# Kernel tuning notes

Measured on AMD Instinct MI355X. Metric: run time of the kernel, lower is better.

The kernel has to match this reference:

```python
import jax, jax.numpy as jnp
import numpy as np

N_NODES = 50000
N_EDGES = 10000
NNZ = 1600000
IN_DIM = 256
OUT_DIM = 128


def setup_inputs() -> dict:
    key = jax.random.key(0)
    k1, k2, k3, k4, k5 = jax.random.split(key, 5)
    X = jax.random.normal(k1, (N_NODES, IN_DIM), dtype=jnp.float32)
    theta = jax.random.normal(k2, (IN_DIM, OUT_DIM), dtype=jnp.float32) * (1.0 / np.sqrt(IN_DIM))
    bias = jax.random.normal(k3, (OUT_DIM,), dtype=jnp.float32) * 0.01
    node_idx = jax.random.randint(k4, (NNZ,), 0, N_NODES, dtype=jnp.int32)
    hyedge_idx = jax.random.randint(k5, (NNZ,), 0, N_EDGES, dtype=jnp.int32)
    return {
        "X": X,
        "theta": theta,
        "bias": bias,
        "node_idx": node_idx,
        "hyedge_idx": hyedge_idx,
        "num_nodes": N_NODES,
        "num_edges": N_EDGES,
    }


def reference(X, theta, bias, node_idx, hyedge_idx, num_nodes, num_edges):
    # Dense transform: [N, in] @ [in, out] -> [N, out]
    Xt = X @ theta
    # MA_v: vertex -> hyperedge aggregation (gather by node_idx, scatter_add by hyedge_idx)
    Y = jax.ops.segment_sum(Xt[node_idx], hyedge_idx, num_segments=num_edges)  # [M, out]
    # MA_e: hyperedge -> vertex aggregation (gather by hyedge_idx, scatter_add by node_idx)
    X_new = jax.ops.segment_sum(Y[hyedge_idx], node_idx, num_segments=num_nodes)  # [N, out]
    # U_v: bias add
    return X_new + bias
```

## Files before the change

### kernel.cpp

```cpp
#include <hip/hip_runtime.h>
#include <hip/hip_bf16.h>

#define NN 50000
#define NE 10000
#define KD 256
#define MD 128

#define NCAP 76

#define RNG 4
#define RDIV 12500
#define ERCAP 96

#define NB_E 313
#define NB_N 196
#define NBT  (NB_E + NB_N)
#define CCAP_E 5760
#define CCAP_N 8960

#define GEMM_BLKS ((NN + 255) / 256)
#define NCB 256
#define CSPAN 6252
#define CPB 6272
#define VIT 4

typedef __attribute__((ext_vector_type(8))) short short8;
typedef __attribute__((ext_vector_type(4))) float f32x4;

union ABfrag { short8 s; unsigned u[4]; };

__device__ inline unsigned pack_bf2(float a, float b) {
    __hip_bfloat162 h = __float22bfloat162_rn(make_float2(a, b));
    return *reinterpret_cast<unsigned*>(&h);
}

__device__ inline unsigned short bf16_1(float a) {
    __hip_bfloat16 h = __float2bfloat16(a);
    return *reinterpret_cast<unsigned short*>(&h);
}

__device__ inline float bf_lo(unsigned v) { return __uint_as_float(v << 16); }
__device__ inline float bf_hi(unsigned v) { return __uint_as_float(v & 0xffff0000u); }

__device__ inline void exscan_block(const int* __restrict__ cnt, int* __restrict__ lst,
                                    int n, int* buf, int tid) {
    int v = (tid < n) ? cnt[tid] : 0;
    buf[tid] = v;
    __syncthreads();
    #pragma unroll
    for (int s = 1; s < 512; s <<= 1) {
        int t = (tid >= s) ? buf[tid - s] : 0;
        __syncthreads();
        buf[tid] += t;
        __syncthreads();
    }
    if (tid < n) lst[tid] = buf[tid] - v;
    __syncthreads();
}

__global__ __launch_bounds__(256) void prep_theta(const float* __restrict__ Th,
                                                  unsigned short* __restrict__ tT,
                                                  int* __restrict__ ccur) {
    int tid = threadIdx.x;
    if (blockIdx.x == 0) { ccur[tid] = 0; ccur[tid + 256] = 0; }
    int gid = blockIdx.x * 256 + tid;
    int k = gid >> 7, c = gid & 127;
    tT[(size_t)c * KD + k] = bf16_1(Th[(size_t)k * MD + c]);
}

__global__ __launch_bounds__(512) void gemm_coarse(const float* __restrict__ X,
                                                   const unsigned short* __restrict__ tT,
                                                   unsigned short* __restrict__ XtU, int N,
                                                   const int* __restrict__ nidx,
                                                   const int* __restrict__ eidx,
                                                   int* __restrict__ ccur,
                                                   unsigned* __restrict__ coarse_e,
                                                   unsigned* __restrict__ coarse_n, int nnz) {
    __shared__ unsigned srt[CPB];
    __shared__ int cnt[NBT], lst[NBT], gb[NBT];
    __shared__ int wsum[8], wpre[8];
    const int tid = threadIdx.x;
    const int wv = tid >> 6, lane = tid & 63;

    if (blockIdx.x >= NCB) {
        const int lr = lane & 15;
        const int lk = lane >> 4;
        const int row0 = (blockIdx.x - NCB) * 256 + wv * 32;
        const int rowA = row0 + lr;
        const int rowB = row0 + 16 + lr;

        f32x4 acc0[8], acc1[8];
        #pragma unroll
        for (int ct = 0; ct < 8; ++ct) {
            acc0[ct] = (f32x4){0.f, 0.f, 0.f, 0.f};
            acc1[ct] = (f32x4){0.f, 0.f, 0.f, 0.f};
        }

        const short8* tTv = (const short8*)tT;
        #pragma unroll
        for (int ks = 0; ks < 8; ++ks) {
            ABfrag a0, a1;
            if (rowA < N) {
                const float* xp = X + (size_t)rowA * KD + ks * 32 + lk * 8;
                float4 v0 = *(const float4*)(xp);
                float4 v1 = *(const float4*)(xp + 4);
                a0.u[0] = pack_bf2(v0.x, v0.y);
                a0.u[1] = pack_bf2(v0.z, v0.w);
                a0.u[2] = pack_bf2(v1.x, v1.y);
                a0.u[3] = pack_bf2(v1.z, v1.w);
            } else a0.u[0] = a0.u[1] = a0.u[2] = a0.u[3] = 0u;
            if (rowB < N) {
                const float* xp = X + (size_t)rowB * KD + ks * 32 + lk * 8;
                float4 v0 = *(const float4*)(xp);
                float4 v1 = *(const float4*)(xp + 4);
                a1.u[0] = pack_bf2(v0.x, v0.y);
                a1.u[1] = pack_bf2(v0.z, v0.w);
                a1.u[2] = pack_bf2(v1.x, v1.y);
                a1.u[3] = pack_bf2(v1.z, v1.w);
            } else a1.u[0] = a1.u[1] = a1.u[2] = a1.u[3] = 0u;

            #pragma unroll
            for (int ct = 0; ct < 8; ++ct) {
                ABfrag b;
                b.s = tTv[(size_t)(ct * 16 + lr) * 32 + ks * 4 + lk];
                acc0[ct] = __builtin_amdgcn_mfma_f32_16x16x32_bf16(a0.s, b.s, acc0[ct], 0, 0, 0);
                acc1[ct] = __builtin_amdgcn_mfma_f32_16x16x32_bf16(a1.s, b.s, acc1[ct], 0, 0, 0);
            }
        }

        #pragma unroll
        for (int ct = 0; ct < 8; ++ct) {
            #pragma unroll
            for (int i = 0; i < 4; ++i) {
                int rA = row0 + lk * 4 + i;
                int rB = row0 + 16 + lk * 4 + i;
                if (rA < N) XtU[(size_t)rA * MD + ct * 16 + lr] = bf16_1(acc0[ct][i]);
                if (rB < N) XtU[(size_t)rB * MD + ct * 16 + lr] = bf16_1(acc1[ct][i]);
            }
        }
        return;
    }

    const int k0 = blockIdx.x * CSPAN;
    int k1 = k0 + CSPAN; if (k1 > nnz) k1 = nnz;
    const int nk = (k1 > k0) ? (k1 - k0) : 0;

    for (int j = tid; j < NBT; j += 512) cnt[j] = 0;
    __syncthreads();

    const int4* e4 = (const int4*)(eidx + k0);
    const int4* n4 = (const int4*)(nidx + k0);
    unsigned rr[VIT * 4];
    #pragma unroll
    for (int it = 0; it < VIT; ++it) {
        int vi = tid + it * 512;
        int base = vi * 4;
        int4 ev = make_int4(0, 0, 0, 0), nv = make_int4(0, 0, 0, 0);
        if (base < nk) { ev = e4[vi]; nv = n4[vi]; }
        #pragma unroll
        for (int j = 0; j < 4; ++j) {
            int e = (j == 0) ? ev.x : (j == 1) ? ev.y : (j == 2) ? ev.z : ev.w;
            int n = (j == 0) ? nv.x : (j == 1) ? nv.y : (j == 2) ? nv.z : nv.w;
            unsigned r = 0u;
            if (base + j < nk) {
                r = ((unsigned)n << 14) | (unsigned)e;
                atomicAdd(&cnt[e >> 5], 1);
                atomicAdd(&cnt[NB_E + (n >> 8)], 1);
            }
            rr[it * 4 + j] = r;
        }
    }
    __syncthreads();

    {
        int myv = (tid < NBT) ? cnt[tid] : 0;
        int v = myv;
        #pragma unroll
        for (int s = 1; s < 64; s <<= 1) {
            int t = __shfl_up(v, s);
            if (lane >= s) v += t;
        }
        if (lane == 63) wsum[wv] = v;
        __syncthreads();
        if (wv == 0) {
            int u = (lane < 8) ? wsum[lane] : 0;
            #pragma unroll
            for (int s = 1; s < 8; s <<= 1) {
                int t = __shfl_up(u, s);
                if (lane >= s) u += t;
            }
            if (lane < 8) wpre[lane] = u - wsum[lane];
        }
        __syncthreads();
        if (tid < NBT) lst[tid] = v - myv + wpre[wv];
        __syncthreads();
    }

    for (int j = tid; j < NBT; j += 512) {
        int c = cnt[j];
        gb[j] = c ? atomicAdd(&ccur[j], c) : 0;
        cnt[j] = 0;
    }
    __syncthreads();

    #pragma unroll
    for (int it = 0; it < VIT; ++it) {
        #pragma unroll
        for (int j = 0; j < 4; ++j) {
            int i = (tid + it * 512) * 4 + j;
            if (i < nk) {
                unsigned r = rr[it * 4 + j];
                int b = (r & 0x3FFF) >> 5;
                int rk = atomicAdd(&cnt[b], 1);
                srt[lst[b] + rk] = r;
            }
        }
    }
    __syncthreads();
    for (int p = tid; p < nk; p += 512) {
        unsigned r = srt[p];
        int b = (r & 0x3FFF) >> 5;
        int g = gb[b] + (p - lst[b]);
        if (g < CCAP_E) coarse_e[(size_t)b * CCAP_E + g] = r;
    }
    __syncthreads();

    #pragma unroll
    for (int it = 0; it < VIT; ++it) {
        #pragma unroll
        for (int j = 0; j < 4; ++j) {
            int i = (tid + it * 512) * 4 + j;
            if (i < nk) {
                unsigned r = rr[it * 4 + j];
                int b = NB_E + ((int)(r >> 14) >> 8);
                int rk = atomicAdd(&cnt[b], 1);
                srt[(lst[b] - nk) + rk] = r;
            }
        }
    }
    __syncthreads();
    for (int p = tid; p < nk; p += 512) {
        unsigned r = srt[p];
        int b = NB_E + ((int)(r >> 14) >> 8);
        int g = gb[b] + (p - (lst[b] - nk));
        if (g < CCAP_N) coarse_n[(size_t)(b - NB_E) * CCAP_N + g] = r;
    }
}

__global__ __launch_bounds__(512) void fine_e(const unsigned* __restrict__ coarse_e,
                                              const int* __restrict__ ccur,
                                              unsigned short* __restrict__ e_slots,
                                              int* __restrict__ e_cnt) {
    __shared__ unsigned srt[CCAP_E];
    __shared__ int cnt[128], lst[128];
    const int tid = threadIdx.x;
    const int b = blockIdx.x;

    const unsigned* buf = coarse_e + (size_t)b * CCAP_E;
    int m = ccur[b]; if (m > CCAP_E) m = CCAP_E;

    for (int j = tid; j < 128; j += 512) cnt[j] = 0;
    __syncthreads();
    for (int i = tid; i < m; i += 512) {
        unsigned r = buf[i];
        int e = r & 0x3FFF;
        int n = (int)(r >> 14);
        atomicAdd(&cnt[((e & 31) << 2) | (n / RDIV)], 1);
    }
    __syncthreads();
    exscan_block(cnt, lst, 128, (int*)srt, tid);
    if (tid < 128) {
        int e = b * 32 + (tid >> 2);
        if (e < NE) {
            int c = cnt[tid]; if (c > ERCAP) c = ERCAP;
            e_cnt[e * RNG + (tid & 3)] = c;
        }
    }
    __syncthreads();
    for (int j = tid; j < 128; j += 512) cnt[j] = 0;
    __syncthreads();
    for (int i = tid; i < m; i += 512) {
        unsigned r = buf[i];
        int e = r & 0x3FFF;
        unsigned n = r >> 14;
        int li = ((e & 31) << 2) | ((int)n / RDIV);
        int rk = atomicAdd(&cnt[li], 1);
        srt[lst[li] + rk] = ((unsigned)li << 16) | n;
    }
    __syncthreads();
    for (int p = tid; p < m; p += 512) {
        unsigned v = srt[p];
        int li = (int)(v >> 16);
        int lr = p - lst[li];
        if (lr < ERCAP) {
            int e = b * 32 + (li >> 2);
            e_slots[((size_t)e * RNG + (li & 3)) * ERCAP + lr] = (unsigned short)(v & 0xFFFF);
        }
    }
}

#define AGG_BLKS ((NE + 7) / 8 * RNG)

__global__ __launch_bounds__(512) void fine_n_agg_ve(const unsigned* __restrict__ coarse_n,
                                                     const int* __restrict__ ccur,
                                                     unsigned short* __restrict__ n_slots,
                                                     int* __restrict__ n_cnt,
                                                     const unsigned* __restrict__ XtB,
                                                     const int* __restrict__ e_cnt,
                                                     const unsigned short* __restrict__ e_slots,
                                                     unsigned* __restrict__ P) {
    __shared__ unsigned srt[CCAP_N];
    __shared__ int cnt[256], lst[256];
    const int tid = threadIdx.x;

    if (blockIdx.x < NB_N) {
        const int bb = blockIdx.x;
        const unsigned* buf = coarse_n + (size_t)bb * CCAP_N;
        int m = ccur[NB_E + bb]; if (m > CCAP_N) m = CCAP_N;

        for (int j = tid; j < 256; j += 512) cnt[j] = 0;
        __syncthreads();
        for (int i = tid; i < m; i += 512) {
            unsigned r = buf[i];
            atomicAdd(&cnt[(r >> 14) & 255], 1);
        }
        __syncthreads();
        exscan_block(cnt, lst, 256, (int*)srt, tid);
        if (tid < 256) {
            int g = bb * 256 + tid;
            if (g < NN) {
                int c = cnt[tid]; if (c > NCAP) c = NCAP;
                n_cnt[g] = c;
            }
        }
        __syncthreads();
        for (int j = tid; j < 256; j += 512) cnt[j] = 0;
        __syncthreads();
        for (int i = tid; i < m; i += 512) {
            unsigned r = buf[i];
            int k = (r >> 14) & 255;
            int rk = atomicAdd(&cnt[k], 1);
            srt[lst[k] + rk] = ((unsigned)k << 16) | (r & 0x3FFF);
        }
        __syncthreads();
        for (int p = tid; p < m; p += 512) {
            unsigned v = srt[p];
            int k = (int)(v >> 16);
            int lr = p - lst[k];
            if (lr < NCAP) {
                int g = bb * 256 + k;
                n_slots[(size_t)g * NCAP + lr] = (unsigned short)(v & 0x3FFF);
            }
        }
        return;
    }

    const int wid = blockIdx.x - NB_N;
    const int r = wid & 3;
    const int g = wid >> 2;
    int wave = g * 8 + (tid >> 6);
    int l    = tid & 63;
    const int grp = l >> 3, sub = l & 7;
    int ec = e_cnt[wave * RNG + r]; if (ec > ERCAP) ec = ERCAP;
    const unsigned short* slots = e_slots + ((size_t)wave * RNG + r) * ERCAP;
    const uint4* Xv = (const uint4*)XtB;

    float a[16];
    #pragma unroll
    for (int i = 0; i < 16; ++i) a[i] = 0.f;

    for (int c = 0; c < ec; c += 64) {
        int m = ec - c; if (m > 64) m = 64;
        int idx = (c + l < ec) ? (int)slots[c + l] : 0;
        for (int j = 0; j < m; j += 8) {
            int mem = j + grp;
            bool valid = mem < m;
            int n = __shfl(idx, valid ? mem : 0);
            const uint4* row = Xv + (size_t)n * 16 + sub * 2;
            uint4 v0 = row[0];
            uint4 v1 = row[1];
            if (valid) {
                a[0]  += bf_lo(v0.x); a[1]  += bf_hi(v0.x);
                a[2]  += bf_lo(v0.y); a[3]  += bf_hi(v0.y);
                a[4]  += bf_lo(v0.z); a[5]  += bf_hi(v0.z);
                a[6]  += bf_lo(v0.w); a[7]  += bf_hi(v0.w);
                a[8]  += bf_lo(v1.x); a[9]  += bf_hi(v1.x);
                a[10] += bf_lo(v1.y); a[11] += bf_hi(v1.y);
                a[12] += bf_lo(v1.z); a[13] += bf_hi(v1.z);
                a[14] += bf_lo(v1.w); a[15] += bf_hi(v1.w);
            }
        }
    }
    #pragma unroll
    for (int i = 0; i < 16; ++i) {
        a[i] += __shfl_xor(a[i], 8);
        a[i] += __shfl_xor(a[i], 16);
        a[i] += __shfl_xor(a[i], 32);
    }
    if (l < 8) {
        uint4 o0 = make_uint4(pack_bf2(a[0],  a[1]),  pack_bf2(a[2],  a[3]),
                              pack_bf2(a[4],  a[5]),  pack_bf2(a[6],  a[7]));
        uint4 o1 = make_uint4(pack_bf2(a[8],  a[9]),  pack_bf2(a[10], a[11]),
                              pack_bf2(a[12], a[13]), pack_bf2(a[14], a[15]));
        uint4* prow = (uint4*)P + ((size_t)r * NE + wave) * 16 + sub * 2;
        prow[0] = o0;
        prow[1] = o1;
    }
}

__global__ __launch_bounds__(256) void reduce_y(const unsigned* __restrict__ P,
                                                unsigned* __restrict__ YB) {
    int gid = blockIdx.x * 256 + threadIdx.x;
    if (gid >= NE * 64) return;
    float a = 0.f, b = 0.f;
    #pragma unroll
    for (int r = 0; r < RNG; ++r) {
        unsigned v = P[(size_t)r * NE * 64 + gid];
        a += bf_lo(v);
        b += bf_hi(v);
    }
    YB[gid] = pack_bf2(a, b);
}

__global__ __launch_bounds__(256) void agg_ev(const unsigned* __restrict__ YB,
                                              const int* __restrict__ n_cnt,
                                              const unsigned short* __restrict__ n_slots,
                                              const float* __restrict__ bias,
                                              float* __restrict__ out) {
    int wave = blockIdx.x * 4 + (threadIdx.x >> 6);
    int l    = threadIdx.x & 63;
    if (wave >= NN) return;
    const int grp = l >> 3, sub = l & 7;
    int cnt = n_cnt[wave]; if (cnt > NCAP) cnt = NCAP;
    const unsigned short* slots = n_slots + (size_t)wave * NCAP;
    const uint4* Yv = (const uint4*)YB;

    float a[16];
    #pragma unroll
    for (int i = 0; i < 16; ++i) a[i] = 0.f;

    for (int c = 0; c < cnt; c += 64) {
        int m = cnt - c; if (m > 64) m = 64;
        int idx = (c + l < cnt) ? (int)slots[c + l] : 0;
        for (int j = 0; j < m; j += 8) {
            int mem = j + grp;
            bool valid = mem < m;
            int e = __shfl(idx, valid ? mem : 0);
            const uint4* row = Yv + (size_t)e * 16 + sub * 2;
            uint4 v0 = row[0];
            uint4 v1 = row[1];
            if (valid) {
                a[0]  += bf_lo(v0.x); a[1]  += bf_hi(v0.x);
                a[2]  += bf_lo(v0.y); a[3]  += bf_hi(v0.y);
                a[4]  += bf_lo(v0.z); a[5]  += bf_hi(v0.z);
                a[6]  += bf_lo(v0.w); a[7]  += bf_hi(v0.w);
                a[8]  += bf_lo(v1.x); a[9]  += bf_hi(v1.x);
                a[10] += bf_lo(v1.y); a[11] += bf_hi(v1.y);
                a[12] += bf_lo(v1.z); a[13] += bf_hi(v1.z);
                a[14] += bf_lo(v1.w); a[15] += bf_hi(v1.w);
            }
        }
    }
    #pragma unroll
    for (int i = 0; i < 16; ++i) {
        a[i] += __shfl_xor(a[i], 8);
        a[i] += __shfl_xor(a[i], 16);
        a[i] += __shfl_xor(a[i], 32);
    }
    if (l < 8) {
        float4* orow = (float4*)(out + (size_t)wave * MD);
        #pragma unroll
        for (int q = 0; q < 4; ++q) {
            float4 bq = ((const float4*)bias)[sub * 4 + q];
            float4 o = make_float4(a[q * 4 + 0] + bq.x, a[q * 4 + 1] + bq.y,
                                   a[q * 4 + 2] + bq.z, a[q * 4 + 3] + bq.w);
            orow[sub * 4 + q] = o;
        }
    }
}

extern "C" void kernel_launch(void* const* d_in, const int* in_sizes, int n_in,
                              void* d_out, int out_size, void* d_ws, size_t ws_size,
                              hipStream_t stream) {
    const float* X     = (const float*)d_in[0];
    const float* theta = (const float*)d_in[1];
    const float* bias  = (const float*)d_in[2];
    const int*   nidx  = (const int*)d_in[3];
    const int*   eidx  = (const int*)d_in[4];
    float*       out   = (float*)d_out;

    const int N   = in_sizes[0] / KD;
    const int nnz = in_sizes[3];

    char* w = (char*)d_ws;
    unsigned*       XtB      = (unsigned*)w;       w += (size_t)NN * MD * 2;
    unsigned*       YB       = (unsigned*)w;       w += (size_t)NE * MD * 2;
    int*            e_cnt    = (int*)w;            w += (size_t)NE * RNG * 4;
    int*            n_cnt    = (int*)w;            w += (size_t)NN * 4;
    int*            ccur     = (int*)w;            w += (size_t)512 * 4;
    unsigned short* thetaT   = (unsigned short*)w; w += (size_t)MD * KD * 2;
    unsigned*       P        = (unsigned*)w;       w += (size_t)RNG * NE * 64 * 4;
    unsigned*       coarse_e = (unsigned*)w;       w += (size_t)NB_E * CCAP_E * 4;
    unsigned*       coarse_n = (unsigned*)w;       w += (size_t)NB_N * CCAP_N * 4;
    unsigned short* e_slots  = (unsigned short*)w; w += (size_t)NE * RNG * ERCAP * 2;
    unsigned short* n_slots  = (unsigned short*)w;

    prep_theta<<<(MD * KD) / 256, 256, 0, stream>>>(theta, thetaT, ccur);

    gemm_coarse<<<NCB + GEMM_BLKS, 512, 0, stream>>>(X, thetaT, (unsigned short*)XtB, N,
                                                     nidx, eidx, ccur,
                                                     coarse_e, coarse_n, nnz);

    fine_e<<<NB_E, 512, 0, stream>>>(coarse_e, ccur, e_slots, e_cnt);

    fine_n_agg_ve<<<NB_N + AGG_BLKS, 512, 0, stream>>>(coarse_n, ccur, n_slots, n_cnt,
                                                       XtB, e_cnt, e_slots, P);

    reduce_y<<<(NE * 64 + 255) / 256, 256, 0, stream>>>(P, YB);

    agg_ev<<<(NN + 3) / 4, 256, 0, stream>>>(YB, n_cnt, n_slots, bias, out);
}
```

Measured before the change: 125.2 us.

## Move node-side coarse binning into the fine_e kernel to rebalance stages

```diff
diff --git a/kernel.cpp b/kernel.cpp
--- a/kernel.cpp
+++ b/kernel.cpp
@@ -24,6 +24,8 @@
 #define CPB 6272
 #define VIT 4
 
+#define AGG_BLKS ((NE + 7) / 8 * RNG)
+
 typedef __attribute__((ext_vector_type(8))) short short8;
 typedef __attribute__((ext_vector_type(4))) float f32x4;
 
@@ -55,6 +57,31 @@
         __syncthreads();
     }
     if (tid < n) lst[tid] = buf[tid] - v;
+    __syncthreads();
+}
+
+__device__ inline void wave_exscan(const int* __restrict__ cnt, int* __restrict__ lst,
+                                   int n, int* wsum, int* wpre, int tid, int wv, int lane) {
+    int myv = (tid < n) ? cnt[tid] : 0;
+    int v = myv;
+    #pragma unroll
+    for (int s = 1; s < 64; s <<= 1) {
+        int t = __shfl_up(v, s);
+        if (lane >= s) v += t;
+    }
+    if (lane == 63) wsum[wv] = v;
+    __syncthreads();
+    if (wv == 0) {
+        int u = (lane < 8) ? wsum[lane] : 0;
+        #pragma unroll
+        for (int s = 1; s < 8; s <<= 1) {
+            int t = __shfl_up(u, s);
+            if (lane >= s) u += t;
+        }
+        if (lane < 8) wpre[lane] = u - wsum[lane];
+    }
+    __syncthreads();
+    if (tid < n) lst[tid] = v - myv + wpre[wv];
     __syncthreads();
 }
 
@@ -68,16 +95,15 @@
     tT[(size_t)c * KD + k] = bf16_1(Th[(size_t)k * MD + c]);
 }
 
-__global__ __launch_bounds__(512) void gemm_coarse(const float* __restrict__ X,
-                                                   const unsigned short* __restrict__ tT,
-                                                   unsigned short* __restrict__ XtU, int N,
-                                                   const int* __restrict__ nidx,
-                                                   const int* __restrict__ eidx,
-                                                   int* __restrict__ ccur,
-                                                   unsigned* __restrict__ coarse_e,
-                                                   unsigned* __restrict__ coarse_n, int nnz) {
+__global__ __launch_bounds__(512) void gemm_coarse_e(const float* __restrict__ X,
+                                                     const unsigned short* __restrict__ tT,
+                                                     unsigned short* __restrict__ XtU, int N,
+                                                     const int* __restrict__ nidx,
+                                                     const int* __restrict__ eidx,
+                                                     int* __restrict__ ccur,
+                                                     unsigned* __restrict__ coarse_e, int nnz) {
     __shared__ unsigned srt[CPB];
-    __shared__ int cnt[NBT], lst[NBT], gb[NBT];
+    __shared__ int cnt[NB_E], lst[NB_E], gb[NB_E];
     __shared__ int wsum[8], wpre[8];
     const int tid = threadIdx.x;
     const int wv = tid >> 6, lane = tid & 63;
@@ -145,7 +171,7 @@
     int k1 = k0 + CSPAN; if (k1 > nnz) k1 = nnz;
     const int nk = (k1 > k0) ? (k1 - k0) : 0;
 
-    for (int j = tid; j < NBT; j += 512) cnt[j] = 0;
+    for (int j = tid; j < NB_E; j += 512) cnt[j] = 0;
     __syncthreads();
 
     const int4* e4 = (const int4*)(eidx + k0);
@@ -165,38 +191,15 @@
             if (base + j < nk) {
                 r = ((unsigned)n << 14) | (unsigned)e;
                 atomicAdd(&cnt[e >> 5], 1);
-                atomicAdd(&cnt[NB_E + (n >> 8)], 1);
             }
             rr[it * 4 + j] = r;
         }
     }
     __syncthreads();
 
-    {
-        int myv = (tid < NBT) ? cnt[tid] : 0;
-        int v = myv;
-        #pragma unroll
-        for (int s = 1; s < 64; s <<= 1) {
-            int t = __shfl_up(v, s);
-            if (lane >= s) v += t;
-        }
-        if (lane == 63) wsum[wv] = v;
-        __syncthreads();
-        if (wv == 0) {
-            int u = (lane < 8) ? wsum[lane] : 0;
-            #pragma unroll
-            for (int s = 1; s < 8; s <<= 1) {
-                int t = __shfl_up(u, s);
-                if (lane >= s) u += t;
-            }
-            if (lane < 8) wpre[lane] = u - wsum[lane];
-        }
-        __syncthreads();
-        if (tid < NBT) lst[tid] = v - myv + wpre[wv];
-        __syncthreads();
-    }
-
-    for (int j = tid; j < NBT; j += 512) {
+    wave_exscan(cnt, lst, NB_E, wsum, wpre, tid, wv, lane);
+
+    for (int j = tid; j < NB_E; j += 512) {
         int c = cnt[j];
         gb[j] = c ? atomicAdd(&ccur[j], c) : 0;
         cnt[j] = 0;
@@ -223,6 +226,104 @@
         int g = gb[b] + (p - lst[b]);
         if (g < CCAP_E) coarse_e[(size_t)b * CCAP_E + g] = r;
     }
+}
+
+__global__ __launch_bounds__(512) void coarse_n_fine_e(const int* __restrict__ nidx,
+                                                       const int* __restrict__ eidx,
+                                                       int* __restrict__ ccur,
+                                                       unsigned* __restrict__ coarse_n,
+                                                       const unsigned* __restrict__ coarse_e,
+                                                       unsigned short* __restrict__ e_slots,
+                                                       int* __restrict__ e_cnt, int nnz) {
+    __shared__ unsigned srt[CPB];
+    __shared__ int cnt[NB_N], lst[NB_N], gb[NB_N];
+    __shared__ int wsum[8], wpre[8];
+    const int tid = threadIdx.x;
+    const int wv = tid >> 6, lane = tid & 63;
+
+    if (blockIdx.x >= NCB) {
+        const int b = blockIdx.x - NCB;
+        const unsigned* buf = coarse_e + (size_t)b * CCAP_E;
+        int m = ccur[b]; if (m > CCAP_E) m = CCAP_E;
+
+        for (int j = tid; j < 128; j += 512) cnt[j] = 0;
+        __syncthreads();
+        for (int i = tid; i < m; i += 512) {
+            unsigned r = buf[i];
+            int e = r & 0x3FFF;
+            int n = (int)(r >> 14);
+            atomicAdd(&cnt[((e & 31) << 2) | (n / RDIV)], 1);
+        }
+        __syncthreads();
+        wave_exscan(cnt, lst, 128, wsum, wpre, tid, wv, lane);
+        if (tid < 128) {
+            int e = b * 32 + (tid >> 2);
+            if (e < NE) {
+                int c = cnt[tid]; if (c > ERCAP) c = ERCAP;
+                e_cnt[e * RNG + (tid & 3)] = c;
+            }
+        }
+        __syncthreads();
+        for (int j = tid; j < 128; j += 512) cnt[j] = 0;
+        __syncthreads();
+        for (int i = tid; i < m; i += 512) {
+            unsigned r = buf[i];
+            int e = r & 0x3FFF;
+            unsigned n = r >> 14;
+            int li = ((e & 31) << 2) | ((int)n / RDIV);
+            int rk = atomicAdd(&cnt[li], 1);
+            srt[lst[li] + rk] = ((unsigned)li << 16) | n;
+        }
+        __syncthreads();
+        for (int p = tid; p < m; p += 512) {
+            unsigned v = srt[p];
+            int li = (int)(v >> 16);
+            int lr = p - lst[li];
+            if (lr < ERCAP) {
+                int e = b * 32 + (li >> 2);
+                e_slots[((size_t)e * RNG + (li & 3)) * ERCAP + lr] = (unsigned short)(v & 0xFFFF);
+            }
+        }
+        return;
+    }
+
+    const int k0 = blockIdx.x * CSPAN;
+    int k1 = k0 + CSPAN; if (k1 > nnz) k1 = nnz;
+    const int nk = (k1 > k0) ? (k1 - k0) : 0;
+
+    for (int j = tid; j < NB_N; j += 512) cnt[j] = 0;
+    __syncthreads();
+
+    const int4* e4 = (const int4*)(eidx + k0);
+    const int4* n4 = (const int4*)(nidx + k0);
+    unsigned rr[VIT * 4];
+    #pragma unroll
+    for (int it = 0; it < VIT; ++it) {
+        int vi = tid + it * 512;
+        int base = vi * 4;
+        int4 ev = make_int4(0, 0, 0, 0), nv = make_int4(0, 0, 0, 0);
+        if (base < nk) { ev = e4[vi]; nv = n4[vi]; }
+        #pragma unroll
+        for (int j = 0; j < 4; ++j) {
+            int e = (j == 0) ? ev.x : (j == 1) ? ev.y : (j == 2) ? ev.z : ev.w;
+            int n = (j == 0) ? nv.x : (j == 1) ? nv.y : (j == 2) ? nv.z : nv.w;
+            unsigned r = 0u;
+            if (base + j < nk) {
+                r = ((unsigned)n << 14) | (unsigned)e;
+                atomicAdd(&cnt[n >> 8], 1);
+            }
+            rr[it * 4 + j] = r;
+        }
+    }
+    __syncthreads();
+
+    wave_exscan(cnt, lst, NB_N, wsum, wpre, tid, wv, lane);
+
+    for (int j = tid; j < NB_N; j += 512) {
+        int c = cnt[j];
+        gb[j] = c ? atomicAdd(&ccur[NB_E + j], c) : 0;
+        cnt[j] = 0;
+    }
     __syncthreads();
 
     #pragma unroll
@@ -232,74 +333,20 @@
             int i = (tid + it * 512) * 4 + j;
             if (i < nk) {
                 unsigned r = rr[it * 4 + j];
-                int b = NB_E + ((int)(r >> 14) >> 8);
+                int b = (int)(r >> 14) >> 8;
                 int rk = atomicAdd(&cnt[b], 1);
-                srt[(lst[b] - nk) + rk] = r;
+                srt[lst[b] + rk] = r;
             }
         }
     }
     __syncthreads();
     for (int p = tid; p < nk; p += 512) {
         unsigned r = srt[p];
-        int b = NB_E + ((int)(r >> 14) >> 8);
-        int g = gb[b] + (p - (lst[b] - nk));
-        if (g < CCAP_N) coarse_n[(size_t)(b - NB_E) * CCAP_N + g] = r;
-    }
-}
-
-__global__ __launch_bounds__(512) void fine_e(const unsigned* __restrict__ coarse_e,
-                                              const int* __restrict__ ccur,
-                                              unsigned short* __restrict__ e_slots,
-                                              int* __restrict__ e_cnt) {
-    __shared__ unsigned srt[CCAP_E];
-    __shared__ int cnt[128], lst[128];
-    const int tid = threadIdx.x;
-    const int b = blockIdx.x;
-
-    const unsigned* buf = coarse_e + (size_t)b * CCAP_E;
-    int m = ccur[b]; if (m > CCAP_E) m = CCAP_E;
-
-    for (int j = tid; j < 128; j += 512) cnt[j] = 0;
-    __syncthreads();
-    for (int i = tid; i < m; i += 512) {
-        unsigned r = buf[i];
-        int e = r & 0x3FFF;
-        int n = (int)(r >> 14);
-        atomicAdd(&cnt[((e & 31) << 2) | (n / RDIV)], 1);
-    }
-    __syncthreads();
-    exscan_block(cnt, lst, 128, (int*)srt, tid);
-    if (tid < 128) {
-        int e = b * 32 + (tid >> 2);
-        if (e < NE) {
-            int c = cnt[tid]; if (c > ERCAP) c = ERCAP;
-            e_cnt[e * RNG + (tid & 3)] = c;
-        }
-    }
-    __syncthreads();
-    for (int j = tid; j < 128; j += 512) cnt[j] = 0;
-    __syncthreads();
-    for (int i = tid; i < m; i += 512) {
-        unsigned r = buf[i];
-        int e = r & 0x3FFF;
-        unsigned n = r >> 14;
-        int li = ((e & 31) << 2) | ((int)n / RDIV);
-        int rk = atomicAdd(&cnt[li], 1);
-        srt[lst[li] + rk] = ((unsigned)li << 16) | n;
-    }
-    __syncthreads();
-    for (int p = tid; p < m; p += 512) {
-        unsigned v = srt[p];
-        int li = (int)(v >> 16);
-        int lr = p - lst[li];
-        if (lr < ERCAP) {
-            int e = b * 32 + (li >> 2);
-            e_slots[((size_t)e * RNG + (li & 3)) * ERCAP + lr] = (unsigned short)(v & 0xFFFF);
-        }
-    }
-}
-
-#define AGG_BLKS ((NE + 7) / 8 * RNG)
+        int b = (int)(r >> 14) >> 8;
+        int g = gb[b] + (p - lst[b]);
+        if (g < CCAP_N) coarse_n[(size_t)b * CCAP_N + g] = r;
+    }
+}
 
 __global__ __launch_bounds__(512) void fine_n_agg_ve(const unsigned* __restrict__ coarse_n,
                                                      const int* __restrict__ ccur,
@@ -507,11 +554,11 @@
 
     prep_theta<<<(MD * KD) / 256, 256, 0, stream>>>(theta, thetaT, ccur);
 
-    gemm_coarse<<<NCB + GEMM_BLKS, 512, 0, stream>>>(X, thetaT, (unsigned short*)XtB, N,
-                                                     nidx, eidx, ccur,
-                                                     coarse_e, coarse_n, nnz);
-
-    fine_e<<<NB_E, 512, 0, stream>>>(coarse_e, ccur, e_slots, e_cnt);
+    gemm_coarse_e<<<NCB + GEMM_BLKS, 512, 0, stream>>>(X, thetaT, (unsigned short*)XtB, N,
+                                                       nidx, eidx, ccur, coarse_e, nnz);
+
+    coarse_n_fine_e<<<NCB + NB_E, 512, 0, stream>>>(nidx, eidx, ccur, coarse_n,
+                                                    coarse_e, e_slots, e_cnt, nnz);
 
     fine_n_agg_ve<<<NB_N + AGG_BLKS, 512, 0, stream>>>(coarse_n, ccur, n_slots, n_cnt,
                                                        XtB, e_cnt, e_slots, P);
```

Result: slower. 132.5 us (+5.9%).
